# Optimization experiments

Hardware: AMD Instinct MI355X
Metric: run time of the kernel (lower is better)

The kernel has to match this reference:

```python
import jax, jax.numpy as jnp
import numpy as np
import math

# static config (see shape_source)
NUM_GRAPHS = 8      # b
L_NODES = 1024      # nodes per graph (uniform -> to_dense_batch is a reshape)
D_INNER = 128
HEADDIM = 16
N_HEADS = D_INNER // HEADDIM  # 8
D_STATE = 64
NUM_DT = 4          # 3 node-dt components + dt_self
AVG_DEG = 16
DIAMETER = 50       # default_graph_diameter
TOL = 0.1
DT_MIN, DT_MAX, DT_FLOOR = 1e-3, 1e-1, 1e-4


def dag_inverse(A):
    """DAGInverse.forward: (I - A)^{-1} via repeated-squaring doubling.
    A: [b, h, l, l]. j = 2^ceil(log2(diameter)); out = prod (I + A^{2^k})."""
    j = 2 ** math.ceil(math.log2(DIAMETER))  # 64
    I = jnp.eye(A.shape[-1], dtype=A.dtype)
    last = A
    out = I + A
    for _ in range(2, int(math.log2(j)) + 1):  # 5 iterations
        last = last @ last
        out = out @ (I + last)
    return out


def setup_inputs() -> dict:
    key = jax.random.key(0)
    k = jax.random.split(key, 8)
    N = NUM_GRAPHS * L_NODES
    x = jax.random.normal(k[0], (N, D_INNER), jnp.float32)
    B_mat = jax.random.normal(k[1], (N, D_STATE), jnp.float32)
    C_mat = jax.random.normal(k[2], (N, D_STATE), jnp.float32)
    dt = jax.random.normal(k[3], (N, NUM_DT * N_HEADS), jnp.float32)
    # dt_bias init as in GraphSSD.__init__
    u = jax.random.uniform(k[4], (N_HEADS,), jnp.float32)
    dt0 = jnp.exp(u * (math.log(DT_MAX) - math.log(DT_MIN)) + math.log(DT_MIN))
    dt0 = jnp.clip(dt0, DT_FLOOR, None)
    dt_bias = dt0 + jnp.log(-jnp.expm1(-dt0))
    D = jnp.ones((N_HEADS,), jnp.float32)
    # edges: per-graph random endpoints, offset to global node ids
    E_per = L_NODES * AVG_DEG
    src_l = jax.random.randint(k[5], (NUM_GRAPHS, E_per), 0, L_NODES)
    dst_l = jax.random.randint(k[6], (NUM_GRAPHS, E_per), 0, L_NODES)
    off = (jnp.arange(NUM_GRAPHS) * L_NODES)[:, None]
    edge_index = jnp.stack([(src_l + off).reshape(-1), (dst_l + off).reshape(-1)], 0).astype(jnp.int32)
    return {"x": x, "B_mat": B_mat, "C_mat": C_mat, "dt": dt,
            "dt_bias": dt_bias, "D": D, "edge_index": edge_index}


def reference(x, B_mat, C_mat, dt, dt_bias, D, edge_index):
    Bn, Lg, H, hd, ds = NUM_GRAPHS, L_NODES, N_HEADS, HEADDIM, D_STATE
    N = Bn * Lg
    # dense batching (uniform graph sizes -> pure reshape, mask all True)
    x_d = x.reshape(Bn, Lg, H, hd).transpose(0, 2, 1, 3)        # b n l h ('(n h)' split)
    B_d = B_mat.reshape(Bn, Lg, ds)                             # broadcast over heads
    C_d = C_mat.reshape(Bn, Lg, ds)
    # dt: 'l (n c) -> c n l'
    dt_c = dt.reshape(N, H, NUM_DT).transpose(2, 1, 0)          # c n l
    dt_node, dt_self = dt_c[:NUM_DT - 1], dt_c[NUM_DT - 1]      # (3,n,N), (n,N)
    dt_self_d = dt_self.T.reshape(Bn, Lg, H).transpose(0, 2, 1)  # b n l
    # multiply_dt_w_A: A = -exp(A_log)= -1 (with_A=False)
    dt_A_node = -jax.nn.softplus(dt_node + dt_bias[None, :, None])  # (3, n, N)
    # edge dt: (dt_s[src] + dt_t[dst]) / 2, then exp
    src, dst = edge_index[0], edge_index[1]
    attr = jnp.exp((dt_A_node[0][:, src] + dt_A_node[1][:, dst]) * 0.5).T  # (E, n)
    # to_dense_adj scatter: [b, l1, l2, h] then -> b h l1 l2
    b_idx, sl, dl = src // Lg, src % Lg, dst % Lg
    A_mat = jnp.zeros((Bn, Lg, Lg, H), x.dtype).at[b_idx, sl, dl].add(attr)
    A_mat = A_mat.transpose(0, 3, 1, 2)                          # b n l1 l2
    # 'leq' normalization with dummy self term
    dt_dummy = jnp.exp(dt_A_node[2]).T.reshape(Bn, Lg, H).transpose(0, 2, 1)  # b n l
    normalizer = A_mat.sum(-1) + dt_dummy                        # b n l1
    A_norm = A_mat / (normalizer[..., None] + TOL)
    # L = (I - A^T)^{-1} via DAGInverse doubling
    Lmat = dag_inverse(jnp.swapaxes(A_norm, -1, -2).astype(jnp.float32))  # b n l t
    L_norm = Lmat * dt_self_d[:, :, None, :]                     # scale along t
    # y = einsum(C, L, B, x); C/B broadcast in heads -> G shared across heads
    G = jnp.einsum('bld,btd->blt', C_d, B_d)[:, None]            # b 1 l t
    y = jnp.einsum('bnlt,bnth->bnlh', L_norm * G, x_d)
    y = y + x_d * D[None, :, None, None]
    # 'b n l h -> b l (h n)'
    y = y.transpose(0, 2, 3, 1).reshape(Bn, Lg, H * hd)
    return y.reshape(N, H * hd)
```

## Files before the change

### kernel.cpp

```cpp
#include <hip/hip_runtime.h>
#include <hip/hip_bf16.h>

#define H_ 8
#define NTOT 8192
#define LG 1024
#define BN 8
#define HD 16
#define DSTATE 64
#define EPG 16384
#define MSZ (1024*1024)

typedef __hip_bfloat16 bf16;
typedef unsigned short ushort_t;
typedef _Float16 f16;
typedef __attribute__((ext_vector_type(8))) _Float16 half8;
typedef __attribute__((ext_vector_type(4))) _Float16 half4;
typedef __attribute__((ext_vector_type(4))) float f4v;

__device__ __forceinline__ float b2f(bf16 v){ return __bfloat162float(v); }
__device__ __forceinline__ float sp_(float z){
  return fmaxf(z, 0.f) + log1pf(expf(-fabsf(z)));
}
__device__ __forceinline__ float ldv(const void* p, size_t i, int f32){
  float v;
  if (f32) v = ((const float*)p)[i];
  else     v = b2f(((const bf16*)p)[i]);
  return v;
}
__device__ __forceinline__ void gl2lds16(const void* g, void* l){
  __builtin_amdgcn_global_load_lds((const __attribute__((address_space(1))) unsigned int*)g,
                                   (__attribute__((address_space(3))) unsigned int*)l,
                                   16, 0, 0);
}

#define BARC() do { asm volatile("" ::: "memory"); __builtin_amdgcn_s_barrier(); asm volatile("" ::: "memory"); } while(0)

__global__ void k_sniff(const void* __restrict__ dt, int* __restrict__ flag){
  const ushort_t* p = (const ushort_t*)dt;
  int tid = threadIdx.x;
  int bad = 0;
  for (int i = tid; i < 512; i += 256){
    int e = (p[i] >> 7) & 0xFF;
    if (e >= 140) bad = 1;
  }
  unsigned long long m = __ballot(bad != 0);
  __shared__ int anybad[4];
  if ((tid & 63) == 0) anybad[tid >> 6] = (m != 0ull) ? 1 : 0;
  __syncthreads();
  if (tid == 0) *flag = (anybad[0] | anybad[1] | anybad[2] | anybad[3]);
}

__global__ void k_nodecoef(const void* __restrict__ dt, const void* __restrict__ dtb,
                           const int* __restrict__ flag,
                           float* __restrict__ a0, float* __restrict__ a1,
                           float* __restrict__ dum, float* __restrict__ sdt){
  int idx = blockIdx.x*256 + threadIdx.x;
  if (idx >= H_*NTOT) return;
  int f32 = *flag;
  int h = idx / NTOT, n = idx - h*NTOT;
  float bias = ldv(dtb, h, f32);
  size_t base = (size_t)n*(4*H_) + h*4;
  float d0, d1, d2, d3;
  if (f32){
    const float* row = (const float*)dt + base;
    d0 = row[0]; d1 = row[1]; d2 = row[2]; d3 = row[3];
  } else {
    const bf16* row = (const bf16*)dt + base;
    d0 = b2f(row[0]); d1 = b2f(row[1]); d2 = b2f(row[2]); d3 = b2f(row[3]);
  }
  a0[(size_t)n*H_ + h] = -sp_(d0 + bias);
  a1[(size_t)n*H_ + h] = -sp_(d1 + bias);
  dum[idx] = expf(-sp_(d2 + bias));
  sdt[idx] = d3;
}

__global__ __launch_bounds__(256) void k_zero(char* base, size_t regB, float* __restrict__ nrm){
  int bh = blockIdx.y;
  if (blockIdx.x < 1024){
    float* Mf = (float*)(base + (size_t)bh*regB) + MSZ;
    int i = blockIdx.x*1024 + threadIdx.x*4;
    *(float4*)(Mf + i) = make_float4(0.f,0.f,0.f,0.f);
  } else {
    int j = threadIdx.x*4;
    *(float4*)(nrm + (size_t)bh*LG + j) = make_float4(0.f,0.f,0.f,0.f);
  }
}

__global__ void k_scatter(const int* __restrict__ ei, const float* __restrict__ a0,
                          const float* __restrict__ a1, char* base, size_t regB,
                          float* __restrict__ nrm,
                          int b0, int h0, int lgHB, int GBp, int nthreads, int Etot){
  int t = blockIdx.x*256 + threadIdx.x;
  if (t >= nthreads) return;
  int HB = 1 << lgHB;
  int hl = t & (HB-1);
  int el = t >> lgHB;
  int e = b0*EPG + el;
  int src = ei[e], dst = ei[Etot + e];
  int g = src >> 10;
  if ((unsigned)(g - b0) >= (unsigned)GBp) return;
  int sl = src & 1023, dl = dst & 1023;
  int h = h0 + hl;
  float attr = expf(0.5f*(a0[(size_t)src*H_ + h] + a1[(size_t)dst*H_ + h]));
  int bhl = (g - b0)*HB + hl;
  float* Mf = (float*)(base + (size_t)bhl*regB) + MSZ;
  atomicAdd(&Mf[(size_t)dl*LG + sl], attr);
  atomicAdd(&nrm[bhl*LG + sl], attr);
}

__global__ __launch_bounds__(256) void k_norm2(char* base, size_t regB,
                            const float* __restrict__ nrm, const float* __restrict__ dum,
                            int b0, int h0, int HB){
  __shared__ ushort_t tb[32][33];
  int bh = blockIdx.z;
  int g = b0 + bh / HB, h = h0 + bh % HB;
  const float* Mf = (const float*)(base + (size_t)bh*regB) + MSZ;
  f16* L0  = (f16*)(base + (size_t)bh*regB);
  f16* L0T = L0 + MSZ;
  f16* O0  = L0 + (size_t)4*MSZ;
  int x0 = blockIdx.x*32, y0 = blockIdx.y*32;
  int tx = threadIdx.x & 31, ty = threadIdx.x >> 5;
  int sl = x0 + tx;
  float denom = nrm[(size_t)bh*LG + sl] + dum[(size_t)h*NTOT + g*LG + sl] + 0.1f;
  float rden = 1.f / denom;
  #pragma unroll
  for (int i = 0; i < 32; i += 8){
    int dl = y0 + ty + i;
    float v = Mf[(size_t)dl*LG + sl] * rden;
    f16 hv = (f16)v;
    L0[(size_t)dl*LG + sl] = hv;
    O0[(size_t)dl*LG + sl] = (f16)(v + (dl == sl ? 1.f : 0.f));
    union { f16 h; ushort_t u; } cv; cv.h = hv;
    tb[tx][ty + i] = cv.u;
  }
  __syncthreads();
  #pragma unroll
  for (int i = 0; i < 32; i += 8){
    union { f16 h; ushort_t u; } cv; cv.u = tb[ty + i][tx];
    L0T[(size_t)(x0 + ty + i)*LG + y0 + tx] = cv.h;
  }
}

__global__ __launch_bounds__(256) void k_G(const void* __restrict__ Bm, const void* __restrict__ Cm,
                                           const int* __restrict__ flag,
                                           f16* __restrict__ G, int b0){
  int gl = blockIdx.z;
  int g = b0 + gl;
  int l0 = blockIdx.y*16, t0 = blockIdx.x*16;
  __shared__ float Cs[16][DSTATE+1];
  __shared__ float Bs[16][DSTATE+1];
  int tid = threadIdx.x;
  int f32 = *flag;
  if (f32){
    const float* Cf = (const float*)Cm;
    const float* Bf = (const float*)Bm;
    for (int i = tid; i < 16*DSTATE; i += 256){
      int r = i >> 6, d = i & 63;
      Cs[r][d] = Cf[(size_t)(g*LG + l0 + r)*DSTATE + d];
      Bs[r][d] = Bf[(size_t)(g*LG + t0 + r)*DSTATE + d];
    }
  } else {
    const bf16* Cb = (const bf16*)Cm;
    const bf16* Bb = (const bf16*)Bm;
    for (int i = tid; i < 16*DSTATE; i += 256){
      int r = i >> 6, d = i & 63;
      Cs[r][d] = b2f(Cb[(size_t)(g*LG + l0 + r)*DSTATE + d]);
      Bs[r][d] = b2f(Bb[(size_t)(g*LG + t0 + r)*DSTATE + d]);
    }
  }
  __syncthreads();
  int r = tid >> 4, c = tid & 15;
  float acc = 0.f;
  #pragma unroll
  for (int d = 0; d < DSTATE; ++d) acc = fmaf(Cs[r][d], Bs[c][d], acc);
  G[(size_t)gl*MSZ + (size_t)(l0+r)*LG + t0 + c] = (f16)acc;
}

__global__ __launch_bounds__(1024, 4) void k_gemm_fused(char* base, size_t regB,
    int nS, int iAs, int iBTs, int iCs, int iCTs,
    int nU, int iAu, int iBTu, int iCu){
  extern __shared__ char lds[];
  int T = nS + nU;
  int s = blockIdx.x + 8*blockIdx.z;
  if (s >= T) return;
  int isS = (s < nS) ? 1 : 0;
  int bh  = isS ? s : (s - nS);
  int iA  = isS ? iAs : iAu;
  int iBT = isS ? iBTs : iBTu;
  int iC  = isS ? iCs : iCu;
  int iCT = isS ? iCTs : -1;
  int addA = 1 - isS;
  char* reg = base + (size_t)bh*regB;
  const f16* Ab = (const f16*)reg + (size_t)iA*MSZ;
  const f16* Bb = (const f16*)reg + (size_t)iBT*MSZ;
  f16* Cb = (f16*)reg + (size_t)iC*MSZ;
  int y = blockIdx.y;
  int i0 = (y >> 2)*256, j0 = (y & 3)*256;
  int tid = threadIdx.x;
  int lane = tid & 63, wv = tid >> 6;
  int wm = wv >> 2, wn = wv & 3;
  int m16 = lane & 15, q = lane >> 4;
  int swz = (q ^ ((m16 >> 1) & 3)) << 4;
  int aoff = (((wm & 1) << 6) + m16)*64 + swz;
  int boff = (((wn & 1) << 6) + m16)*64 + swz;
  int tl = tid & 511;
  int sr = tl >> 2;
  int sc = (tl & 3) ^ ((sr >> 1) & 3);

  auto ISSUE2 = [&](int hA){
    if (hA >= 128) return;
    int h = (tid < 512) ? hA : (hA + 1);
    int j = h & 3;
    int kt2 = h >> 2;
    const f16* M = (j < 2) ? Ab : Bb;
    int rb = ((j < 2) ? i0 : j0) + ((j & 1) << 7);
    const f16* src = M + (size_t)(rb + sr)*LG + kt2*32 + sc*8;
    char* dst = lds + ((h & 15) << 13) + tl*16;
    gl2lds16(src, dst);
  };

  ISSUE2(0); ISSUE2(2);
  ISSUE2(4); ISSUE2(6);
  ISSUE2(8); ISSUE2(10);
  f4v acc[4][4] = {};
  half8 af[4], bfr[4];
  asm volatile("s_waitcnt vmcnt(4)" ::: "memory");
  BARC();

  for (int kt = 0; kt < 32; ++kt){
    int sb = (kt & 3) << 2;
    const char* Asl = lds + ((sb + (wm >> 1)) << 13);
    const char* Bsl = lds + ((sb + 2 + (wn >> 1)) << 13);
    #pragma unroll
    for (int t = 0; t < 4; ++t) af[t]  = *(const half8*)(Asl + aoff + t*1024);
    #pragma unroll
    for (int t = 0; t < 4; ++t) bfr[t] = *(const half8*)(Bsl + boff + t*1024);
    int hn = 4*(kt + 3);
    ISSUE2(hn); ISSUE2(hn + 2);
    asm volatile("s_waitcnt lgkmcnt(0)" ::: "memory");
    __builtin_amdgcn_s_setprio(1);
    #pragma unroll
    for (int mt = 0; mt < 4; ++mt)
      #pragma unroll
      for (int nt = 0; nt < 4; ++nt)
        acc[mt][nt] = __builtin_amdgcn_mfma_f32_16x16x32_f16(af[mt], bfr[nt], acc[mt][nt], 0, 0, 0);
    __builtin_amdgcn_s_setprio(0);
    if (kt <= 28)      asm volatile("s_waitcnt vmcnt(4)" ::: "memory");
    else if (kt == 29) asm volatile("s_waitcnt vmcnt(2)" ::: "memory");
    else if (kt == 30) asm volatile("s_waitcnt vmcnt(0)" ::: "memory");
    BARC();
  }

  f16* CT = (f16*)reg + (size_t)((iCT < 0) ? iC : iCT)*MSZ;
  #pragma unroll
  for (int mt = 0; mt < 4; ++mt){
    #pragma unroll
    for (int nt = 0; nt < 4; ++nt){
      int gr0 = i0 + wm*64 + mt*16 + q*4;
      int gc  = j0 + wn*64 + nt*16 + m16;
      half4 tv;
      #pragma unroll
      for (int r = 0; r < 4; ++r){
        float v = acc[mt][nt][r];
        if (addA) v += (float)Ab[(size_t)(gr0 + r)*LG + gc];
        f16 hv = (f16)v;
        tv[r] = hv;
        Cb[(size_t)(gr0 + r)*LG + gc] = hv;
      }
      if (iCT >= 0)
        *(half4*)&CT[(size_t)gc*LG + gr0] = tv;
    }
  }
}

__global__ __launch_bounds__(256) void k_final2(char* base, size_t regB, int iO,
    const f16* __restrict__ Gh, const float* __restrict__ sdt,
    const void* __restrict__ x, const void* __restrict__ Dv,
    const int* __restrict__ flag, void* __restrict__ out,
    int b0, int h0, int HB){
  __shared__ float coef[16][257];
  int bh = blockIdx.y;
  int gl = bh / HB, g = b0 + gl, h = h0 + bh % HB;
  int L0r = blockIdx.x*16;
  int tid = threadIdx.x;
  int lr = tid >> 4, ts = tid & 15;
  int f32 = *flag;
  const f16* Orow = (const f16*)(base + (size_t)bh*regB) + (size_t)iO*MSZ + (size_t)(L0r+lr)*LG;
  const f16* Grow = Gh + (size_t)gl*MSZ + (size_t)(L0r+lr)*LG;
  const float* srow = sdt + (size_t)h*NTOT + g*LG;
  float acc = 0.f;
  for (int tc = 0; tc < LG; tc += 256){
    int tb = tc + ts*16;
    __syncthreads();
    half8 o0 = *(const half8*)&Orow[tb];
    half8 o1 = *(const half8*)&Orow[tb + 8];
    half8 g0 = *(const half8*)&Grow[tb];
    half8 g1 = *(const half8*)&Grow[tb + 8];
    #pragma unroll
    for (int j = 0; j < 8; ++j){
      coef[lr][ts*16 + j]     = (float)o0[j] * (float)g0[j] * srow[tb + j];
      coef[lr][ts*16 + 8 + j] = (float)o1[j] * (float)g1[j] * srow[tb + 8 + j];
    }
    __syncthreads();
    if (f32){
      const float* xf = (const float*)x + (size_t)(g*LG + tc)*128 + h*HD + ts;
      for (int t = 0; t < 256; ++t)
        acc = fmaf(coef[lr][t], xf[(size_t)t*128], acc);
    } else {
      const bf16* xb = (const bf16*)x + (size_t)(g*LG + tc)*128 + h*HD + ts;
      for (int t = 0; t < 256; ++t)
        acc = fmaf(coef[lr][t], b2f(xb[(size_t)t*128]), acc);
    }
  }
  int l = L0r + lr, d = ts;
  float xs = ldv(x, (size_t)(g*LG + l)*128 + h*HD + d, f32);
  float dv = ldv(Dv, h, f32);
  float v = acc + xs*dv;
  size_t off = (size_t)(g*LG + l)*128 + d*H_ + h;
  if (f32) ((float*)out)[off] = v;
  else     ((bf16*)out)[off] = __float2bfloat16(v);
}

extern "C" void kernel_launch(void* const* d_in, const int* in_sizes, int n_in,
                              void* d_out, int out_size, void* d_ws, size_t ws_size,
                              hipStream_t stream){
  const void* x   = d_in[0];
  const void* Bm  = d_in[1];
  const void* Cm  = d_in[2];
  const void* dt  = d_in[3];
  const void* dtb = d_in[4];
  const void* Dv  = d_in[5];
  const int*  ei  = (const int*)d_in[6];
  int Etot = in_sizes[6] / 2;

  static int attrDone = 0;
  if (!attrDone){
    hipFuncSetAttribute(reinterpret_cast<const void*>(k_gemm_fused),
                        hipFuncAttributeMaxDynamicSharedMemorySize, 131072);
    attrDone = 1;
  }

  const size_t REG = (size_t)6*MSZ*2;
  int GB = 1, HB = 1;
  const int cfgs[7][2] = {{8,8},{4,8},{2,8},{1,8},{1,4},{1,2},{1,1}};
  for (int i = 0; i < 7; ++i){
    int gb = cfgs[i][0], hb = cfgs[i][1];
    size_t need = 4ull*(4ull*H_*NTOT + 64)
                + 4ull*(size_t)gb*hb*LG
                + 2ull*(size_t)gb*MSZ
                + (size_t)gb*hb*REG;
    if (need <= ws_size){ GB = gb; HB = hb; break; }
  }
  int lgHB = (HB==8)?3:((HB==4)?2:((HB==2)?1:0));
  int nbh = GB*HB;

  float* a0  = (float*)d_ws;
  float* a1  = a0 + H_*NTOT;
  float* dum = a1 + H_*NTOT;
  float* sdt = dum + H_*NTOT;
  int*  flag = (int*)(sdt + H_*NTOT);
  float* nrm = (float*)flag + 64;
  f16* G     = (f16*)(nrm + (size_t)nbh*LG);
  char* chainBase = (char*)(G + (size_t)GB*MSZ);

  k_sniff<<<1, 256, 0, stream>>>(dt, flag);
  k_nodecoef<<<(H_*NTOT + 255)/256, 256, 0, stream>>>(dt, dtb, flag, a0, a1, dum, sdt);

  for (int b0 = 0; b0 < BN; b0 += GB){
    for (int h0 = 0; h0 < H_; h0 += HB){
      k_zero<<<dim3(1025, nbh), 256, 0, stream>>>(chainBase, REG, nrm);
      int nthr = GB*EPG*HB;
      k_scatter<<<(nthr + 255)/256, 256, 0, stream>>>(ei, a0, a1, chainBase, REG, nrm,
                                                      b0, h0, lgHB, GB, nthr, Etot);
      k_norm2<<<dim3(32, 32, nbh), 256, 0, stream>>>(chainBase, REG, nrm, dum, b0, h0, HB);
      if (h0 == 0){
        dim3 gg(64, 64, GB);
        k_G<<<gg, 256, 0, stream>>>(Bm, Cm, flag, G, b0);
      }
      int lA = 0, lAT = 1, lC = 2, lCT = 3, oA = 4, oC = 5;
      {
        int T = nbh;
        dim3 gg(8, 16, (T + 7)/8);
        k_gemm_fused<<<gg, 1024, 131072, stream>>>(chainBase, REG, nbh, lA, lAT, lC, lCT,
                                                   0, 0, 0, 0);
      }
      for (int k = 0; k < 4; ++k){
        int T = 2*nbh;
        dim3 gg(8, 16, (T + 7)/8);
        k_gemm_fused<<<gg, 1024, 131072, stream>>>(chainBase, REG,
                                                   nbh, lC, lCT, lA, lAT,
                                                   nbh, oA, lCT, oC);
        int tp;
        tp = lA; lA = lC; lC = tp;
        tp = lAT; lAT = lCT; lCT = tp;
        tp = oA; oA = oC; oC = tp;
      }
      {
        int T = nbh;
        dim3 gg(8, 16, (T + 7)/8);
        k_gemm_fused<<<gg, 1024, 131072, stream>>>(chainBase, REG, 0, 0, 0, 0, 0,
                                                   nbh, oA, lCT, oC);
        int tp = oA; oA = oC; oC = tp;
      }
      dim3 fg(64, nbh);
      k_final2<<<fg, 256, 0, stream>>>(chainBase, REG, oA, G, sdt, x, Dv, flag, d_out, b0, h0, HB);
    }
  }
}
```

Baseline: 2.258 ms.

## Stagger wave groups in GEMM main loop with inline-asm LDS reads

Splits the 16 waves of the fp16 GEMM block into two groups. One group reads LDS fragments and then does its MFMAs; the other prefetches the next k-tile's fragments after its MFMAs, so LDS reads and matrix math from different waves interleave. LDS reads now use inline-asm ds_read_b128 with immediate offsets and sched_barriers, and the vmcnt waits are tightened by one stage. This risks LDS hazards: group-1 waves read the next tile before the barrier, which is only safe if the load-wait accounting still guarantees that tile has arrived.

Measured after the change: 2.965 ms. 31.3% more time.

```diff
diff --git a/kernel.cpp b/kernel.cpp
--- a/kernel.cpp
+++ b/kernel.cpp
@@ -32,8 +32,13 @@
                                    (__attribute__((address_space(3))) unsigned int*)l,
                                    16, 0, 0);
 }
+__device__ __forceinline__ unsigned ldsaddr(const void* p){
+  return (unsigned)(uintptr_t)(__attribute__((address_space(3))) const char*)p;
+}
 
 #define BARC() do { asm volatile("" ::: "memory"); __builtin_amdgcn_s_barrier(); asm volatile("" ::: "memory"); } while(0)
+#define SB0() __builtin_amdgcn_sched_barrier(0)
+#define DSR(dst, base, off) asm volatile("ds_read_b128 %0, %1 offset:" #off : "=v"(dst) : "v"(base))
 
 __global__ void k_sniff(const void* __restrict__ dt, int* __restrict__ flag){
   const ushort_t* p = (const ushort_t*)dt;
@@ -218,38 +223,67 @@
     char* dst = lds + ((h & 15) << 13) + tl*16;
     gl2lds16(src, dst);
   };
+  unsigned lbase = ldsaddr(lds);
+  auto ADDRA = [&](int tk){ return lbase + (unsigned)(((((tk & 3) << 2) + (wm >> 1)) << 13)) + (unsigned)aoff; };
+  auto ADDRB = [&](int tk){ return lbase + (unsigned)(((((tk & 3) << 2) + 2 + (wn >> 1)) << 13)) + (unsigned)boff; };
+
+  #define READ8(tk) do { \
+    unsigned aA = ADDRA(tk), aB = ADDRB(tk); \
+    DSR(bf0, aB, 0); DSR(bf1, aB, 1024); DSR(bf2, aB, 2048); DSR(bf3, aB, 3072); \
+    DSR(af0, aA, 0); DSR(af1, aA, 1024); DSR(af2, aA, 2048); DSR(af3, aA, 3072); } while(0)
+  #define MFMA16() do { \
+    acc[0][0] = __builtin_amdgcn_mfma_f32_16x16x32_f16(af0, bf0, acc[0][0], 0, 0, 0); \
+    acc[0][1] = __builtin_amdgcn_mfma_f32_16x16x32_f16(af0, bf1, acc[0][1], 0, 0, 0); \
+    acc[0][2] = __builtin_amdgcn_mfma_f32_16x16x32_f16(af0, bf2, acc[0][2], 0, 0, 0); \
+    acc[0][3] = __builtin_amdgcn_mfma_f32_16x16x32_f16(af0, bf3, acc[0][3], 0, 0, 0); \
+    acc[1][0] = __builtin_amdgcn_mfma_f32_16x16x32_f16(af1, bf0, acc[1][0], 0, 0, 0); \
+    acc[1][1] = __builtin_amdgcn_mfma_f32_16x16x32_f16(af1, bf1, acc[1][1], 0, 0, 0); \
+    acc[1][2] = __builtin_amdgcn_mfma_f32_16x16x32_f16(af1, bf2, acc[1][2], 0, 0, 0); \
+    acc[1][3] = __builtin_amdgcn_mfma_f32_16x16x32_f16(af1, bf3, acc[1][3], 0, 0, 0); \
+    acc[2][0] = __builtin_amdgcn_mfma_f32_16x16x32_f16(af2, bf0, acc[2][0], 0, 0, 0); \
+    acc[2][1] = __builtin_amdgcn_mfma_f32_16x16x32_f16(af2, bf1, acc[2][1], 0, 0, 0); \
+    acc[2][2] = __builtin_amdgcn_mfma_f32_16x16x32_f16(af2, bf2, acc[2][2], 0, 0, 0); \
+    acc[2][3] = __builtin_amdgcn_mfma_f32_16x16x32_f16(af2, bf3, acc[2][3], 0, 0, 0); \
+    acc[3][0] = __builtin_amdgcn_mfma_f32_16x16x32_f16(af3, bf0, acc[3][0], 0, 0, 0); \
+    acc[3][1] = __builtin_amdgcn_mfma_f32_16x16x32_f16(af3, bf1, acc[3][1], 0, 0, 0); \
+    acc[3][2] = __builtin_amdgcn_mfma_f32_16x16x32_f16(af3, bf2, acc[3][2], 0, 0, 0); \
+    acc[3][3] = __builtin_amdgcn_mfma_f32_16x16x32_f16(af3, bf3, acc[3][3], 0, 0, 0); } while(0)
 
   ISSUE2(0); ISSUE2(2);
   ISSUE2(4); ISSUE2(6);
   ISSUE2(8); ISSUE2(10);
   f4v acc[4][4] = {};
-  half8 af[4], bfr[4];
-  asm volatile("s_waitcnt vmcnt(4)" ::: "memory");
+  half8 af0, af1, af2, af3, bf0, bf1, bf2, bf3;
+  asm volatile("s_waitcnt vmcnt(2)" ::: "memory");
   BARC();
+  int g1 = wv >> 3;
+  if (g1){ READ8(0); }
 
   for (int kt = 0; kt < 32; ++kt){
-    int sb = (kt & 3) << 2;
-    const char* Asl = lds + ((sb + (wm >> 1)) << 13);
-    const char* Bsl = lds + ((sb + 2 + (wn >> 1)) << 13);
-    #pragma unroll
-    for (int t = 0; t < 4; ++t) af[t]  = *(const half8*)(Asl + aoff + t*1024);
-    #pragma unroll
-    for (int t = 0; t < 4; ++t) bfr[t] = *(const half8*)(Bsl + boff + t*1024);
     int hn = 4*(kt + 3);
-    ISSUE2(hn); ISSUE2(hn + 2);
-    asm volatile("s_waitcnt lgkmcnt(0)" ::: "memory");
-    __builtin_amdgcn_s_setprio(1);
-    #pragma unroll
-    for (int mt = 0; mt < 4; ++mt)
-      #pragma unroll
-      for (int nt = 0; nt < 4; ++nt)
-        acc[mt][nt] = __builtin_amdgcn_mfma_f32_16x16x32_f16(af[mt], bfr[nt], acc[mt][nt], 0, 0, 0);
-    __builtin_amdgcn_s_setprio(0);
-    if (kt <= 28)      asm volatile("s_waitcnt vmcnt(4)" ::: "memory");
-    else if (kt == 29) asm volatile("s_waitcnt vmcnt(2)" ::: "memory");
-    else if (kt == 30) asm volatile("s_waitcnt vmcnt(0)" ::: "memory");
+    if (!g1){
+      READ8(kt);
+      ISSUE2(hn); ISSUE2(hn + 2);
+      asm volatile("s_waitcnt lgkmcnt(0)"); SB0();
+      __builtin_amdgcn_s_setprio(1);
+      MFMA16();
+      __builtin_amdgcn_s_setprio(0);
+      SB0();
+    } else {
+      asm volatile("s_waitcnt lgkmcnt(0)"); SB0();
+      __builtin_amdgcn_s_setprio(1);
+      MFMA16();
+      __builtin_amdgcn_s_setprio(0);
+      SB0();
+      if (kt < 31){ READ8(kt + 1); }
+      ISSUE2(hn); ISSUE2(hn + 2);
+    }
+    if (kt <= 28)      asm volatile("s_waitcnt vmcnt(2)" ::: "memory");
+    else if (kt == 29) asm volatile("s_waitcnt vmcnt(0)" ::: "memory");
     BARC();
   }
+  #undef READ8
+  #undef MFMA16
 
   f16* CT = (f16*)reg + (size_t)((iCT < 0) ? iC : iCT)*MSZ;
   #pragma unroll
```
